# Kernel optimization log

Measured on AMD Instinct MI355X. Metric: run time of the kernel, lower is better.

The kernel has to match this reference:

```python
import jax, jax.numpy as jnp
import numpy as np


def _affine_mats(thetas, lambda1s, lambda2s, H, W):
    # Replicates torch.stack(rows, dim=1) then stack(dim=2): the 'rows' end up as COLUMNS,
    # exactly matching the original module's construction.
    z = jnp.zeros_like(lambda1s)
    o = jnp.ones_like(lambda1s)
    scale = jnp.stack([jnp.stack([lambda1s, z, z], 1),
                       jnp.stack([z, lambda2s, z], 1),
                       jnp.stack([z, z, o], 1)], axis=2)  # [B,3,3]
    th = -thetas
    rot = jnp.stack([jnp.stack([jnp.cos(th), jnp.sin(th), z], 1),
                     jnp.stack([-jnp.sin(th), jnp.cos(th), z], 1),
                     jnp.stack([z, z, o], 1)], axis=2)
    trans = jnp.stack([jnp.stack([o, z, o * W], 1),
                       jnp.stack([z, o, o * H], 1),
                       jnp.stack([z, z, o], 1)], axis=2)
    fw = rot @ trans                       # forward_warp
    fws = scale @ fw                       # forward_warp_scaled
    overall = jnp.linalg.inv(jnp.linalg.inv(fw) @ fws)
    return overall[:, 0:2, :]              # [B,2,3]


def _affine_grid(theta, H, W):
    # torch affine_grid, align_corners=False: normalized pixel-center coords in [-1,1]
    xs = (jnp.arange(W, dtype=theta.dtype) + 0.5) * (2.0 / W) - 1.0
    ys = (jnp.arange(H, dtype=theta.dtype) + 0.5) * (2.0 / H) - 1.0
    X, Y = jnp.meshgrid(xs, ys)                        # [H,W]
    base = jnp.stack([X, Y, jnp.ones_like(X)], -1)     # [H,W,3]
    return jnp.einsum('bij,hwj->bhwi', theta, base)    # [B,H,W,2] (x,y)


def _grid_sample_bilinear_zeros(x, grid):
    # torch grid_sample(mode='bilinear', padding_mode='zeros', align_corners=False)
    B, C, H, W = x.shape
    gx = (grid[..., 0] + 1.0) * (W * 0.5) - 0.5        # [B,H,W] source pixel coords
    gy = (grid[..., 1] + 1.0) * (H * 0.5) - 0.5
    x0 = jnp.floor(gx); y0 = jnp.floor(gy)
    x1 = x0 + 1.0;      y1 = y0 + 1.0
    wx1 = gx - x0; wx0 = 1.0 - wx1
    wy1 = gy - y0; wy0 = 1.0 - wy1
    x0i = x0.astype(jnp.int32); x1i = x1.astype(jnp.int32)
    y0i = y0.astype(jnp.int32); y1i = y1.astype(jnp.int32)
    b_idx = jnp.arange(B)[:, None, None]

    def gather(yi, xi):
        yc = jnp.clip(yi, 0, H - 1)
        xc = jnp.clip(xi, 0, W - 1)
        v = x[b_idx, :, yc, xc]                        # [B,H,W,C]
        m = ((yi >= 0) & (yi < H) & (xi >= 0) & (xi < W)).astype(x.dtype)
        return v * m[..., None]

    out = (gather(y0i, x0i) * (wy0 * wx0)[..., None]
           + gather(y0i, x1i) * (wy0 * wx1)[..., None]
           + gather(y1i, x0i) * (wy1 * wx0)[..., None]
           + gather(y1i, x1i) * (wy1 * wx1)[..., None])  # [B,H,W,C]
    return jnp.transpose(out, (0, 3, 1, 2))            # [B,C,H,W]


def setup_inputs() -> dict:
    key = jax.random.key(0)
    k1, k2, k3, k4 = jax.random.split(key, 4)
    B, C, H, W = 32, 3, 512, 512
    return {
        'x': jax.random.normal(k1, (B, C, H, W), dtype=jnp.float32),
        'thetas': jax.random.normal(k2, (B,), dtype=jnp.float32),
        'lambda1s': jax.random.uniform(k3, (B,), dtype=jnp.float32),
        'lambda2s': jax.random.uniform(k4, (B,), dtype=jnp.float32),
    }


def reference(x, thetas, lambda1s, lambda2s):
    H, W = x.shape[2], x.shape[3]
    theta = _affine_mats(thetas, lambda1s, lambda2s, H, W)   # [B,2,3]
    grid = _affine_grid(theta, H, W)                         # [B,H,W,2]
    return _grid_sample_bilinear_zeros(x, grid).astype(jnp.float32)
```

## Files before the change

### kernel.cpp

```cpp
#include <hip/hip_runtime.h>
#include <math.h>

constexpr int B = 32;
constexpr int C = 3;
constexpr int H = 512;
constexpr int W = 512;
constexpr int HW = H * W;

__global__ __launch_bounds__(256)
void warp_kernel(const float* __restrict__ x,
                 const float* __restrict__ thetas,
                 const float* __restrict__ l1s,
                 const float* __restrict__ l2s,
                 float* __restrict__ out) {
    const int lid  = blockIdx.x;
    const int xcd  = lid & 7;
    const int slot = lid >> 3;
    const int b    = xcd + ((slot >> 8) << 3);
    const int hb   = slot & 255;

    __shared__ float sc[4];
    if (threadIdx.x == 0) {
        double th = -(double)thetas[b];
        double c = cos(th), s = sin(th);
        double a = 1.0 / (double)l1s[b];
        double d = 1.0 / (double)l2s[b];
        sc[0] = (float)(a * c * c + d * s * s);
        sc[1] = (float)(c * s * (d - a));
        sc[2] = sc[1];
        sc[3] = (float)(a * s * s + d * c * c);
    }
    __syncthreads();
    const float t00 = sc[0], t01 = sc[1], t10 = sc[2], t11 = sc[3];

    const int tid   = threadIdx.x;
    const int lane  = tid & 63;
    const int wv    = tid >> 6;
    const int h     = (hb << 1) | (wv >> 1);
    const int wbase = (wv & 1) << 8;

    const float Y = ((float)h + 0.5f) * (2.0f / (float)H) - 1.0f;

    int   row0[4], row1[4];
    bool  xeq[4];
    float w00[4], w01[4], w10[4], w11[4];
    bool any_valid = false;

    #pragma unroll
    for (int j = 0; j < 4; ++j) {
        const int w = wbase + (j << 6) + lane;
        const float X = ((float)w + 0.5f) * (2.0f / (float)W) - 1.0f;
        const float gx = (t00 * X + t01 * Y + 1.0f) * ((float)W * 0.5f) - 0.5f;
        const float gy = (t10 * X + t11 * Y + 1.0f) * ((float)H * 0.5f) - 0.5f;

        const float x0f = floorf(gx), y0f = floorf(gy);
        const float wx1 = gx - x0f, wx0 = 1.0f - wx1;
        const float wy1 = gy - y0f, wy0 = 1.0f - wy1;

        const int x0 = (int)x0f, y0 = (int)y0f;
        const int x1 = x0 + 1,  y1 = y0 + 1;

        const bool vx0 = ((unsigned)x0 < (unsigned)W);
        const bool vx1 = ((unsigned)x1 < (unsigned)W);
        const bool vy0 = ((unsigned)y0 < (unsigned)H);
        const bool vy1 = ((unsigned)y1 < (unsigned)H);

        const int xbj = min(max(x0, 0), W - 2);
        xeq[j] = (x0 == xbj);

        row0[j] = min(max(y0, 0), H - 1) * W + xbj;
        row1[j] = min(max(y1, 0), H - 1) * W + xbj;

        w00[j] = (vy0 && vx0) ? wy0 * wx0 : 0.0f;
        w01[j] = (vy0 && vx1) ? wy0 * wx1 : 0.0f;
        w10[j] = (vy1 && vx0) ? wy1 * wx0 : 0.0f;
        w11[j] = (vy1 && vx1) ? wy1 * wx1 : 0.0f;

        any_valid = any_valid || ((vy0 || vy1) && (vx0 || vx1));
    }

    float r[C][4];
    #pragma unroll
    for (int ch = 0; ch < C; ++ch)
        #pragma unroll
        for (int j = 0; j < 4; ++j) r[ch][j] = 0.0f;

    if (any_valid) {
        const float* __restrict__ base = x + (size_t)b * C * HW;
        #pragma unroll
        for (int j = 0; j < 4; ++j) {
            float2 a0[C], a1[C];
            #pragma unroll
            for (int ch = 0; ch < C; ++ch) {
                a0[ch] = *reinterpret_cast<const float2*>(base + ch * HW + row0[j]);
                a1[ch] = *reinterpret_cast<const float2*>(base + ch * HW + row1[j]);
            }
            #pragma unroll
            for (int ch = 0; ch < C; ++ch) {
                const float v00 = xeq[j] ? a0[ch].x : a0[ch].y;
                const float v01 = xeq[j] ? a0[ch].y : a0[ch].x;
                const float v10 = xeq[j] ? a1[ch].x : a1[ch].y;
                const float v11 = xeq[j] ? a1[ch].y : a1[ch].x;
                r[ch][j] = v00 * w00[j] + v01 * w01[j] + v10 * w10[j] + v11 * w11[j];
            }
        }
    }

    const size_t obase = (size_t)b * C * HW + (size_t)h * W + (size_t)wbase + lane;
    #pragma unroll
    for (int ch = 0; ch < C; ++ch) {
        #pragma unroll
        for (int j = 0; j < 4; ++j) {
            out[obase + (size_t)ch * HW + (j << 6)] = r[ch][j];
        }
    }
}

extern "C" void kernel_launch(void* const* d_in, const int* in_sizes, int n_in,
                              void* d_out, int out_size, void* d_ws, size_t ws_size,
                              hipStream_t stream) {
    const float* x      = (const float*)d_in[0];
    const float* thetas = (const float*)d_in[1];
    const float* l1s    = (const float*)d_in[2];
    const float* l2s    = (const float*)d_in[3];
    float* out          = (float*)d_out;

    warp_kernel<<<dim3((H / 2) * B), 256, 0, stream>>>(x, thetas, l1s, l2s, out);
}
```

Baseline: 207.2 us.

## Map one output pixel per thread with 2D grid and predicated row loads

```diff
diff --git a/kernel.cpp b/kernel.cpp
--- a/kernel.cpp
+++ b/kernel.cpp
@@ -13,11 +13,7 @@
                  const float* __restrict__ l1s,
                  const float* __restrict__ l2s,
                  float* __restrict__ out) {
-    const int lid  = blockIdx.x;
-    const int xcd  = lid & 7;
-    const int slot = lid >> 3;
-    const int b    = xcd + ((slot >> 8) << 3);
-    const int hb   = slot & 255;
+    const int b = blockIdx.y;
 
     __shared__ float sc[4];
     if (threadIdx.x == 0) {
@@ -33,86 +29,68 @@
     __syncthreads();
     const float t00 = sc[0], t01 = sc[1], t10 = sc[2], t11 = sc[3];
 
-    const int tid   = threadIdx.x;
-    const int lane  = tid & 63;
-    const int wv    = tid >> 6;
-    const int h     = (hb << 1) | (wv >> 1);
-    const int wbase = (wv & 1) << 8;
+    const int h = blockIdx.x >> 1;
+    const int w = ((blockIdx.x & 1) << 8) | threadIdx.x;
 
     const float Y = ((float)h + 0.5f) * (2.0f / (float)H) - 1.0f;
+    const float X = ((float)w + 0.5f) * (2.0f / (float)W) - 1.0f;
+    const float gx = (t00 * X + t01 * Y + 1.0f) * ((float)W * 0.5f) - 0.5f;
+    const float gy = (t10 * X + t11 * Y + 1.0f) * ((float)H * 0.5f) - 0.5f;
 
-    int   row0[4], row1[4];
-    bool  xeq[4];
-    float w00[4], w01[4], w10[4], w11[4];
-    bool any_valid = false;
+    const float x0f = floorf(gx), y0f = floorf(gy);
+    const float wx1 = gx - x0f, wx0 = 1.0f - wx1;
+    const float wy1 = gy - y0f, wy0 = 1.0f - wy1;
 
+    const int x0 = (int)x0f, y0 = (int)y0f;
+    const int x1 = x0 + 1,  y1 = y0 + 1;
+
+    const bool vx0 = ((unsigned)x0 < (unsigned)W);
+    const bool vx1 = ((unsigned)x1 < (unsigned)W);
+    const bool vy0 = ((unsigned)y0 < (unsigned)H);
+    const bool vy1 = ((unsigned)y1 < (unsigned)H);
+
+    const int xb  = min(max(x0, 0), W - 2);
+    const bool xeq = (x0 == xb);
+    const bool anyx = vx0 || vx1;
+    const bool pr0 = vy0 && anyx;
+    const bool pr1 = vy1 && anyx;
+
+    const int row0 = min(max(y0, 0), H - 1) * W + xb;
+    const int row1 = min(max(y1, 0), H - 1) * W + xb;
+
+    const float w00 = wy0 * wx0, w01 = wy0 * wx1;
+    const float w10 = wy1 * wx0, w11 = wy1 * wx1;
+
+    float r[C];
     #pragma unroll
-    for (int j = 0; j < 4; ++j) {
-        const int w = wbase + (j << 6) + lane;
-        const float X = ((float)w + 0.5f) * (2.0f / (float)W) - 1.0f;
-        const float gx = (t00 * X + t01 * Y + 1.0f) * ((float)W * 0.5f) - 0.5f;
-        const float gy = (t10 * X + t11 * Y + 1.0f) * ((float)H * 0.5f) - 0.5f;
+    for (int ch = 0; ch < C; ++ch) r[ch] = 0.0f;
 
-        const float x0f = floorf(gx), y0f = floorf(gy);
-        const float wx1 = gx - x0f, wx0 = 1.0f - wx1;
-        const float wy1 = gy - y0f, wy0 = 1.0f - wy1;
+    if (pr0 || pr1) {
+        const float* __restrict__ base = x + (size_t)b * C * HW;
 
-        const int x0 = (int)x0f, y0 = (int)y0f;
-        const int x1 = x0 + 1,  y1 = y0 + 1;
+        float2 a0[C], a1[C];
+        #pragma unroll
+        for (int ch = 0; ch < C; ++ch) {
+            a0[ch] = make_float2(0.0f, 0.0f);
+            a1[ch] = make_float2(0.0f, 0.0f);
+            if (pr0) a0[ch] = *reinterpret_cast<const float2*>(base + ch * HW + row0);
+            if (pr1) a1[ch] = *reinterpret_cast<const float2*>(base + ch * HW + row1);
+        }
 
-        const bool vx0 = ((unsigned)x0 < (unsigned)W);
-        const bool vx1 = ((unsigned)x1 < (unsigned)W);
-        const bool vy0 = ((unsigned)y0 < (unsigned)H);
-        const bool vy1 = ((unsigned)y1 < (unsigned)H);
-
-        const int xbj = min(max(x0, 0), W - 2);
-        xeq[j] = (x0 == xbj);
-
-        row0[j] = min(max(y0, 0), H - 1) * W + xbj;
-        row1[j] = min(max(y1, 0), H - 1) * W + xbj;
-
-        w00[j] = (vy0 && vx0) ? wy0 * wx0 : 0.0f;
-        w01[j] = (vy0 && vx1) ? wy0 * wx1 : 0.0f;
-        w10[j] = (vy1 && vx0) ? wy1 * wx0 : 0.0f;
-        w11[j] = (vy1 && vx1) ? wy1 * wx1 : 0.0f;
-
-        any_valid = any_valid || ((vy0 || vy1) && (vx0 || vx1));
-    }
-
-    float r[C][4];
-    #pragma unroll
-    for (int ch = 0; ch < C; ++ch)
         #pragma unroll
-        for (int j = 0; j < 4; ++j) r[ch][j] = 0.0f;
-
-    if (any_valid) {
-        const float* __restrict__ base = x + (size_t)b * C * HW;
-        #pragma unroll
-        for (int j = 0; j < 4; ++j) {
-            float2 a0[C], a1[C];
-            #pragma unroll
-            for (int ch = 0; ch < C; ++ch) {
-                a0[ch] = *reinterpret_cast<const float2*>(base + ch * HW + row0[j]);
-                a1[ch] = *reinterpret_cast<const float2*>(base + ch * HW + row1[j]);
-            }
-            #pragma unroll
-            for (int ch = 0; ch < C; ++ch) {
-                const float v00 = xeq[j] ? a0[ch].x : a0[ch].y;
-                const float v01 = xeq[j] ? a0[ch].y : a0[ch].x;
-                const float v10 = xeq[j] ? a1[ch].x : a1[ch].y;
-                const float v11 = xeq[j] ? a1[ch].y : a1[ch].x;
-                r[ch][j] = v00 * w00[j] + v01 * w01[j] + v10 * w10[j] + v11 * w11[j];
-            }
+        for (int ch = 0; ch < C; ++ch) {
+            const float v00 = vx0 ? (xeq ? a0[ch].x : a0[ch].y) : 0.0f;
+            const float v01 = vx1 ? (xeq ? a0[ch].y : a0[ch].x) : 0.0f;
+            const float v10 = vx0 ? (xeq ? a1[ch].x : a1[ch].y) : 0.0f;
+            const float v11 = vx1 ? (xeq ? a1[ch].y : a1[ch].x) : 0.0f;
+            r[ch] = v00 * w00 + v01 * w01 + v10 * w10 + v11 * w11;
         }
     }
 
-    const size_t obase = (size_t)b * C * HW + (size_t)h * W + (size_t)wbase + lane;
+    const size_t obase = (size_t)b * C * HW + (size_t)h * W + w;
     #pragma unroll
     for (int ch = 0; ch < C; ++ch) {
-        #pragma unroll
-        for (int j = 0; j < 4; ++j) {
-            out[obase + (size_t)ch * HW + (j << 6)] = r[ch][j];
-        }
+        out[obase + (size_t)ch * HW] = r[ch];
     }
 }
 
@@ -125,5 +103,5 @@
     const float* l2s    = (const float*)d_in[3];
     float* out          = (float*)d_out;
 
-    warp_kernel<<<dim3((H / 2) * B), 256, 0, stream>>>(x, thetas, l1s, l2s, out);
+    warp_kernel<<<dim3(H * 2, B), 256, 0, stream>>>(x, thetas, l1s, l2s, out);
 }
```

New measurement: 190.4 us. -8.1%, faster.
